# Performance work log

Hardware: AMD Instinct MI355X
Metric: run time of the kernel (lower is better)

## Reference

```python
import jax, jax.numpy as jnp
import numpy as np

N_NODES = 50000
N_EDGES = 800000
N_GRAPHS = 64
IN_CH = 128
HID = [64, 128]
MLP_CH = [128, 64, 64, 64, 1]


def _glorot(key, fan_in, fan_out):
    lim = jnp.sqrt(6.0 / (fan_in + fan_out))
    return jax.random.uniform(key, (fan_in, fan_out), jnp.float32, -lim, lim)


def setup_inputs() -> dict:
    key = jax.random.key(0)
    ks = jax.random.split(key, 16)
    x = jax.random.normal(ks[0], (N_NODES, IN_CH), jnp.float32)
    edge_index = jax.random.randint(ks[1], (2, N_EDGES), 0, N_NODES, jnp.int64)
    batch = jnp.sort(jax.random.randint(ks[2], (N_NODES,), 0, N_GRAPHS, jnp.int64))
    inp = {"x": x, "edge_index": edge_index, "batch": batch}
    # GCNConv weights (x @ W + b)
    inp["W1"] = _glorot(ks[3], IN_CH, HID[0]);  inp["b1"] = jnp.zeros((HID[0],), jnp.float32)
    inp["W2"] = _glorot(ks[4], HID[0], HID[1]); inp["b2"] = jnp.zeros((HID[1],), jnp.float32)
    # MLP weights
    for i in range(4):
        inp[f"M{i+1}"] = _glorot(ks[5 + i], MLP_CH[i], MLP_CH[i + 1])
        inp[f"c{i+1}"] = jnp.zeros((MLP_CH[i + 1],), jnp.float32)
    return inp


def _gcn_conv(x, src, dst, dinv, W, b):
    # x' = D^-1/2 (A + I) D^-1/2 (x W) + b, via gather-scale-scatter over edges
    h = x @ W                                   # [N, F]
    norm = dinv[src] * dinv[dst]                # [E+N]
    msg = h[src] * norm[:, None]                # gather + scale
    out = jax.ops.segment_sum(msg, dst, num_segments=x.shape[0])
    return out + b


def reference(x, edge_index, batch, W1, b1, W2, b2, M1, c1, M2, c2, M3, c3, M4, c4):
    N = x.shape[0]
    x = x.astype(jnp.float32)
    # add self loops (PyG GCNConv default)
    loops = jnp.arange(N, dtype=edge_index.dtype)
    src = jnp.concatenate([edge_index[0], loops])
    dst = jnp.concatenate([edge_index[1], loops])
    deg = jax.ops.segment_sum(jnp.ones_like(src, jnp.float32), dst, num_segments=N)
    dinv = jnp.where(deg > 0, jax.lax.rsqrt(jnp.maximum(deg, 1.0)), 0.0)

    h = jax.nn.relu(_gcn_conv(x, src, dst, dinv, W1, b1))
    h = jax.nn.relu(_gcn_conv(h, src, dst, dinv, W2, b2))

    # global mean pool per graph
    sums = jax.ops.segment_sum(h, batch, num_segments=N_GRAPHS)
    cnts = jax.ops.segment_sum(jnp.ones((N,), jnp.float32), batch, num_segments=N_GRAPHS)
    g = sums / jnp.maximum(cnts, 1.0)[:, None]   # [G, 128]

    # MLP (eval mode: dropout is identity)
    g = jax.nn.leaky_relu(g @ M1 + c1, negative_slope=0.2)
    g = jax.nn.leaky_relu(g @ M2 + c2, negative_slope=0.1)
    g = jax.nn.leaky_relu(g @ M3 + c3, negative_slope=0.1)
    g = jax.nn.relu(g @ M4 + c4)
    return g
```

## Files before the change

### kernel.cpp

```cpp
#include <hip/hip_runtime.h>
#include <hip/hip_fp16.h>

#define N_NODES 50000
#define N_EDGES 800000
#define N_GRAPHS 64

#define CAP 64
#define FILL_STRIPES 256

struct __align__(8)  h4v { __half2 a, b; };
struct __align__(16) h8v { __half2 a, b, c, d; };


__global__ void k_init(int* __restrict__ cnt, float* __restrict__ sums,
                       const float* __restrict__ W2, __half* __restrict__ w2h,
                       const int* __restrict__ batch, int* __restrict__ gend) {
    int i = blockIdx.x * 256 + threadIdx.x;
    if (i < N_NODES) {
        cnt[i] = 0;
        if (i == N_NODES - 1 || batch[i] != batch[i + 1]) gend[batch[i]] = i + 1;
    }
    if (i < N_GRAPHS * 128) sums[i] = 0.f;
    if (i < 64 * 128) w2h[i] = __float2half_rn(W2[i]);
}


__global__ void k_fill_direct(const int* __restrict__ src, const int* __restrict__ dst,
                              int* __restrict__ cnt, unsigned short* __restrict__ csr, int E) {
    const int range = blockIdx.x & 7;
    const int stripe = blockIdx.x >> 3;
    const int lo = range * (N_NODES / 8);
    const int hi = lo + (N_NODES / 8);
    for (int e = stripe * 256 + threadIdx.x; e < E; e += FILL_STRIPES * 256) {
        int d = dst[e];
        if (d >= lo && d < hi) {
            int slot = atomicAdd(&cnt[d], 1);
            if (slot < CAP) csr[(size_t)d * CAP + slot] = (unsigned short)src[e];
        }
    }
}


__global__ __launch_bounds__(256) void k_gemm1(const float* __restrict__ A,
                                               const float* __restrict__ W,
                                               const int* __restrict__ cnt,
                                               __half* __restrict__ Cout, int N) {
    const int FIN = 128;
    __shared__ __align__(16) float As[64 * (FIN + 2)];
    __shared__ __align__(16) float Wsm[FIN * 64];
    const int t = threadIdx.x;
    const int row0 = blockIdx.x * 64;

    const int NF4 = 64 * FIN / 4;
    for (int idx = t; idx < NF4; idx += 256) {
        int r = idx / (FIN / 4);
        int c4 = idx % (FIN / 4);
        float4 v = make_float4(0.f, 0.f, 0.f, 0.f);
        if (row0 + r < N) v = ((const float4*)(A + (size_t)(row0 + r) * FIN))[c4];
        float* p = &As[r * (FIN + 2) + c4 * 4];
        ((float2*)p)[0] = make_float2(v.x, v.y);
        ((float2*)p)[1] = make_float2(v.z, v.w);
    }
    for (int idx = t; idx < FIN * 16; idx += 256) {
        int r = idx / 16, c4 = idx % 16;
        *((float4*)&Wsm[r * 64 + c4 * 4]) = ((const float4*)(W + (size_t)r * 64))[c4];
    }
    __syncthreads();

    const int tc = (t & 15) * 4;
    const int tr = (t >> 4) * 4;
    float acc[4][4] = {};
#pragma unroll 4
    for (int k = 0; k < FIN; k += 2) {
        float2 a[4];
#pragma unroll
        for (int r = 0; r < 4; ++r)
            a[r] = *(const float2*)&As[(tr + r) * (FIN + 2) + k];
        float4 w0 = *(const float4*)&Wsm[k * 64 + tc];
        float4 w1 = *(const float4*)&Wsm[(k + 1) * 64 + tc];
#pragma unroll
        for (int r = 0; r < 4; ++r) {
            acc[r][0] = fmaf(a[r].x, w0.x, acc[r][0]);
            acc[r][1] = fmaf(a[r].x, w0.y, acc[r][1]);
            acc[r][2] = fmaf(a[r].x, w0.z, acc[r][2]);
            acc[r][3] = fmaf(a[r].x, w0.w, acc[r][3]);
            acc[r][0] = fmaf(a[r].y, w1.x, acc[r][0]);
            acc[r][1] = fmaf(a[r].y, w1.y, acc[r][1]);
            acc[r][2] = fmaf(a[r].y, w1.z, acc[r][2]);
            acc[r][3] = fmaf(a[r].y, w1.w, acc[r][3]);
        }
    }

#pragma unroll
    for (int r = 0; r < 4; ++r) {
        int row = row0 + tr + r;
        if (row < N) {
            float s = rsqrtf((float)(min(cnt[row], CAP) + 1));
            __half2* dsth = (__half2*)(Cout + (size_t)row * 64 + tc);
            dsth[0] = __floats2half2_rn(acc[r][0] * s, acc[r][1] * s);
            dsth[1] = __floats2half2_rn(acc[r][2] * s, acc[r][3] * s);
        }
    }
}


template <bool RELU>
__global__ void k_agg(const h8v* __restrict__ h, const int* __restrict__ cnt,
                      const unsigned short* __restrict__ csr,
                      const float* __restrict__ bias, h8v* __restrict__ out, int N) {
    int node = blockIdx.x * 32 + (threadIdx.x >> 3);
    int lane = threadIdx.x & 7;
    if (node >= N) return;
    int c = min(cnt[node], CAP);
    float di = rsqrtf((float)(c + 1));
    h8v sv = h[(size_t)node * 8 + lane];
    float2 p0 = __half22float2(sv.a), p1 = __half22float2(sv.b);
    float2 p2 = __half22float2(sv.c), p3 = __half22float2(sv.d);
    float f0 = p0.x, f1 = p0.y, f2 = p1.x, f3 = p1.y;
    float f4 = p2.x, f5 = p2.y, f6 = p3.x, f7 = p3.y;
    float g0 = 0, g1 = 0, g2 = 0, g3 = 0, g4 = 0, g5 = 0, g6 = 0, g7 = 0;
    const unsigned short* row = csr + (size_t)node * CAP;
    int j = 0;
    for (; j + 4 <= c; j += 4) {
        ushort4 s4 = *(const ushort4*)(row + j);
        h8v v0 = h[(size_t)s4.x * 8 + lane];
        h8v v1 = h[(size_t)s4.y * 8 + lane];
        h8v v2 = h[(size_t)s4.z * 8 + lane];
        h8v v3 = h[(size_t)s4.w * 8 + lane];
        float2 a0 = __half22float2(v0.a), a1 = __half22float2(v0.b),
               a2 = __half22float2(v0.c), a3 = __half22float2(v0.d);
        float2 b0 = __half22float2(v1.a), b1 = __half22float2(v1.b),
               b2 = __half22float2(v1.c), b3 = __half22float2(v1.d);
        f0 += a0.x; f1 += a0.y; f2 += a1.x; f3 += a1.y;
        f4 += a2.x; f5 += a2.y; f6 += a3.x; f7 += a3.y;
        g0 += b0.x; g1 += b0.y; g2 += b1.x; g3 += b1.y;
        g4 += b2.x; g5 += b2.y; g6 += b3.x; g7 += b3.y;
        float2 c0 = __half22float2(v2.a), c1 = __half22float2(v2.b),
               c2 = __half22float2(v2.c), c3 = __half22float2(v2.d);
        float2 d0 = __half22float2(v3.a), d1 = __half22float2(v3.b),
               d2 = __half22float2(v3.c), d3 = __half22float2(v3.d);
        f0 += c0.x; f1 += c0.y; f2 += c1.x; f3 += c1.y;
        f4 += c2.x; f5 += c2.y; f6 += c3.x; f7 += c3.y;
        g0 += d0.x; g1 += d0.y; g2 += d1.x; g3 += d1.y;
        g4 += d2.x; g5 += d2.y; g6 += d3.x; g7 += d3.y;
    }
    for (; j < c; ++j) {
        h8v v = h[(size_t)row[j] * 8 + lane];
        float2 a0 = __half22float2(v.a), a1 = __half22float2(v.b),
               a2 = __half22float2(v.c), a3 = __half22float2(v.d);
        f0 += a0.x; f1 += a0.y; f2 += a1.x; f3 += a1.y;
        f4 += a2.x; f5 += a2.y; f6 += a3.x; f7 += a3.y;
    }
    float s0 = f0 + g0, s1 = f1 + g1, s2 = f2 + g2, s3 = f3 + g3;
    float s4 = f4 + g4, s5 = f5 + g5, s6 = f6 + g6, s7 = f7 + g7;
    h8v o;
    if (RELU) {
        float4 bv0 = ((const float4*)bias)[lane * 2];
        float4 bv1 = ((const float4*)bias)[lane * 2 + 1];
        float r0 = fmaf(s0, di, bv0.x); r0 = r0 > 0.f ? r0 : 0.f;
        float r1 = fmaf(s1, di, bv0.y); r1 = r1 > 0.f ? r1 : 0.f;
        float r2 = fmaf(s2, di, bv0.z); r2 = r2 > 0.f ? r2 : 0.f;
        float r3 = fmaf(s3, di, bv0.w); r3 = r3 > 0.f ? r3 : 0.f;
        float r4 = fmaf(s4, di, bv1.x); r4 = r4 > 0.f ? r4 : 0.f;
        float r5 = fmaf(s5, di, bv1.y); r5 = r5 > 0.f ? r5 : 0.f;
        float r6 = fmaf(s6, di, bv1.z); r6 = r6 > 0.f ? r6 : 0.f;
        float r7 = fmaf(s7, di, bv1.w); r7 = r7 > 0.f ? r7 : 0.f;
        o.a = __floats2half2_rn(di * r0, di * r1);
        o.b = __floats2half2_rn(di * r2, di * r3);
        o.c = __floats2half2_rn(di * r4, di * r5);
        o.d = __floats2half2_rn(di * r6, di * r7);
    } else {
        o.a = __floats2half2_rn(s0 * di, s1 * di);
        o.b = __floats2half2_rn(s2 * di, s3 * di);
        o.c = __floats2half2_rn(s4 * di, s5 * di);
        o.d = __floats2half2_rn(s6 * di, s7 * di);
    }
    out[(size_t)node * 8 + lane] = o;
}


__global__ __launch_bounds__(256) void k_gemm_pool128(
    const __half2* __restrict__ A2,
    const __half2* __restrict__ w2h,
    const float* __restrict__ bias,
    const int* __restrict__ batch,
    float* __restrict__ sums, int N) {
    __shared__ __align__(16) float As[64 * 66];
    __shared__ __align__(16) __half2 Wh[64 * 64];
    __shared__ float red[8][132];
    __shared__ int batchLDS[64];
    const int t = threadIdx.x;
    const int row0 = blockIdx.x * 64;

    for (int idx = t; idx < 4096; idx += 256) Wh[idx] = w2h[idx];
    if (t < 64) batchLDS[t] = batch[min(row0 + t, N - 1)];
    for (int idx = t; idx < 64 * 32; idx += 256) {
        int r = idx >> 5, c2 = idx & 31;
        float2 v = make_float2(0.f, 0.f);
        if (row0 + r < N) v = __half22float2(A2[(size_t)(row0 + r) * 32 + c2]);
        *(float2*)&As[r * 66 + c2 * 2] = v;
    }
    __syncthreads();

    const int tc = (t & 31) * 4;
    const int tr = (t >> 5) * 8;
    float acc[8][4] = {};
#pragma unroll 4
    for (int k = 0; k < 64; k += 2) {
        float2 a[8];
#pragma unroll
        for (int r = 0; r < 8; ++r)
            a[r] = *(const float2*)&As[(tr + r) * 66 + k];
        h4v wv0 = *(const h4v*)&Wh[k * 64 + (tc >> 1)];
        h4v wv1 = *(const h4v*)&Wh[(k + 1) * 64 + (tc >> 1)];
        float2 w00 = __half22float2(wv0.a), w01 = __half22float2(wv0.b);
        float2 w10 = __half22float2(wv1.a), w11 = __half22float2(wv1.b);
#pragma unroll
        for (int r = 0; r < 8; ++r) {
            acc[r][0] = fmaf(a[r].x, w00.x, acc[r][0]);
            acc[r][1] = fmaf(a[r].x, w00.y, acc[r][1]);
            acc[r][2] = fmaf(a[r].x, w01.x, acc[r][2]);
            acc[r][3] = fmaf(a[r].x, w01.y, acc[r][3]);
            acc[r][0] = fmaf(a[r].y, w10.x, acc[r][0]);
            acc[r][1] = fmaf(a[r].y, w10.y, acc[r][1]);
            acc[r][2] = fmaf(a[r].y, w11.x, acc[r][2]);
            acc[r][3] = fmaf(a[r].y, w11.y, acc[r][3]);
        }
    }

    float4 bv = *(const float4*)&bias[tc];
    float v[8][4];
#pragma unroll
    for (int r = 0; r < 8; ++r) {
        bool valid = (row0 + tr + r) < N;
        v[r][0] = valid ? fmaxf(acc[r][0] + bv.x, 0.f) : 0.f;
        v[r][1] = valid ? fmaxf(acc[r][1] + bv.y, 0.f) : 0.f;
        v[r][2] = valid ? fmaxf(acc[r][2] + bv.z, 0.f) : 0.f;
        v[r][3] = valid ? fmaxf(acc[r][3] + bv.w, 0.f) : 0.f;
    }

    const int g0 = batchLDS[0], g1 = batchLDS[63];
    const int rg = t >> 5;
    for (int g = g0; g <= g1; ++g) {
        float p0 = 0.f, p1 = 0.f, p2 = 0.f, p3 = 0.f;
#pragma unroll
        for (int r = 0; r < 8; ++r) {
            if (batchLDS[tr + r] == g) { p0 += v[r][0]; p1 += v[r][1]; p2 += v[r][2]; p3 += v[r][3]; }
        }
        red[rg][tc + 0] = p0; red[rg][tc + 1] = p1;
        red[rg][tc + 2] = p2; red[rg][tc + 3] = p3;
        __syncthreads();
        for (int off = 4; off > 0; off >>= 1) {
            if (rg < off) {
#pragma unroll
                for (int c = 0; c < 4; ++c) red[rg][tc + c] += red[rg + off][tc + c];
            }
            __syncthreads();
        }
        if (rg == 0) {
#pragma unroll
            for (int c = 0; c < 4; ++c)
                atomicAdd(&sums[g * 128 + tc + c], red[0][tc + c]);
        }
        __syncthreads();
    }
}


__global__ void k_mlp(const float* __restrict__ sums, const int* __restrict__ gend,
                      const float* __restrict__ M1, const float* __restrict__ c1,
                      const float* __restrict__ M2, const float* __restrict__ c2,
                      const float* __restrict__ M3, const float* __restrict__ c3,
                      const float* __restrict__ M4, const float* __restrict__ c4,
                      float* __restrict__ out) {
    __shared__ float g[128], t1[64], t2[64], t3[64];
    __shared__ float cntb;
    int b = blockIdx.x;
    int t = threadIdx.x;
    if (t == 0) {
        int lb = (b > 0) ? gend[b - 1] : 0;
        cntb = fmaxf((float)(gend[b] - lb), 1.0f);
    }
    __syncthreads();
    if (t < 128) g[t] = sums[b * 128 + t] / cntb;
    __syncthreads();
    if (t < 64) {
        float acc = c1[t];
        for (int k = 0; k < 128; ++k) acc = fmaf(g[k], M1[k * 64 + t], acc);
        t1[t] = acc >= 0.f ? acc : 0.2f * acc;
    }
    __syncthreads();
    if (t < 64) {
        float acc = c2[t];
        for (int k = 0; k < 64; ++k) acc = fmaf(t1[k], M2[k * 64 + t], acc);
        t2[t] = acc >= 0.f ? acc : 0.1f * acc;
    }
    __syncthreads();
    if (t < 64) {
        float acc = c3[t];
        for (int k = 0; k < 64; ++k) acc = fmaf(t2[k], M3[k * 64 + t], acc);
        t3[t] = acc >= 0.f ? acc : 0.1f * acc;
    }
    __syncthreads();
    if (t == 0) {
        float acc = c4[0];
        for (int k = 0; k < 64; ++k) acc = fmaf(t3[k], M4[k], acc);
        out[b] = fmaxf(acc, 0.f);
    }
}


extern "C" void kernel_launch(void* const* d_in, const int* in_sizes, int n_in,
                              void* d_out, int out_size, void* d_ws, size_t ws_size,
                              hipStream_t stream) {
    const float* x   = (const float*)d_in[0];
    const int*   ei  = (const int*)d_in[1];
    const int*   bat = (const int*)d_in[2];
    const float* W1  = (const float*)d_in[3];
    const float* b1  = (const float*)d_in[4];
    const float* W2  = (const float*)d_in[5];
    const float* b2  = (const float*)d_in[6];
    const float* M1  = (const float*)d_in[7];
    const float* c1  = (const float*)d_in[8];
    const float* M2  = (const float*)d_in[9];
    const float* c2  = (const float*)d_in[10];
    const float* M3  = (const float*)d_in[11];
    const float* c3  = (const float*)d_in[12];
    const float* M4  = (const float*)d_in[13];
    const float* c4  = (const float*)d_in[14];
    float* out = (float*)d_out;

    const int* src = ei;
    const int* dst = ei + N_EDGES;

    float* bufA    = (float*)d_ws;
    float* bufB    = bufA + (size_t)N_NODES * 64;
    float* sums    = bufB + (size_t)N_NODES * 64;
    int*   cnt     = (int*)(sums + N_GRAPHS * 128);
    unsigned short* csr = (unsigned short*)(cnt + N_NODES);
    __half* w2h    = (__half*)(csr + (size_t)N_NODES * CAP);
    int*   gend    = (int*)(w2h + 64 * 128);

    k_init<<<(N_NODES + 255) / 256, 256, 0, stream>>>(cnt, sums, W2, w2h, bat, gend);
    k_fill_direct<<<8 * FILL_STRIPES, 256, 0, stream>>>(src, dst, cnt, csr, N_EDGES);

    const int NBLK = (N_NODES + 63) / 64;
    const int ABLK = (N_NODES + 31) / 32;

    k_gemm1<<<NBLK, 256, 0, stream>>>(x, W1, cnt, (__half*)bufA, N_NODES);
    k_agg<true><<<ABLK, 256, 0, stream>>>(
        (const h8v*)bufA, cnt, csr, b1, (h8v*)bufB, N_NODES);

    k_agg<false><<<ABLK, 256, 0, stream>>>(
        (const h8v*)bufB, cnt, csr, nullptr, (h8v*)bufA, N_NODES);
    k_gemm_pool128<<<NBLK, 256, 0, stream>>>(
        (const __half2*)bufA, (const __half2*)w2h, b2, bat, sums, N_NODES);

    k_mlp<<<N_GRAPHS, 128, 0, stream>>>(sums, gend,
                                        M1, c1, M2, c2, M3, c3, M4, c4, out);
}
```

Before: 216.2 us.

## Fuse init with CSR fill and pooling with MLP via cooperative grid sync

Merges the init kernel and the edge-fill kernel into one cooperative kernel that separates the two phases with a grid-wide sync. It also merges the GEMM-plus-pool kernel with the MLP head, so the first 64 blocks run the MLP after a grid sync. This removes two kernel launches and their inter-kernel gaps. In exchange it adds grid-barrier overhead and depends on every block being co-resident, which the launch-bounds occupancy hints are meant to guarantee; if that fails, the cooperative launch fails.

```diff
diff --git a/kernel.cpp b/kernel.cpp
--- a/kernel.cpp
+++ b/kernel.cpp
@@ -1,37 +1,41 @@
 #include <hip/hip_runtime.h>
 #include <hip/hip_fp16.h>
+#include <hip/hip_cooperative_groups.h>
+
+namespace cg = cooperative_groups;
 
 #define N_NODES 50000
 #define N_EDGES 800000
 #define N_GRAPHS 64
 
 #define CAP 64
-#define FILL_STRIPES 256
+#define BUILD_BLOCKS 2048
 
 struct __align__(8)  h4v { __half2 a, b; };
 struct __align__(16) h8v { __half2 a, b, c, d; };
 
 
-__global__ void k_init(int* __restrict__ cnt, float* __restrict__ sums,
-                       const float* __restrict__ W2, __half* __restrict__ w2h,
-                       const int* __restrict__ batch, int* __restrict__ gend) {
-    int i = blockIdx.x * 256 + threadIdx.x;
-    if (i < N_NODES) {
-        cnt[i] = 0;
-        if (i == N_NODES - 1 || batch[i] != batch[i + 1]) gend[batch[i]] = i + 1;
-    }
-    if (i < N_GRAPHS * 128) sums[i] = 0.f;
-    if (i < 64 * 128) w2h[i] = __float2half_rn(W2[i]);
-}
-
-
-__global__ void k_fill_direct(const int* __restrict__ src, const int* __restrict__ dst,
-                              int* __restrict__ cnt, unsigned short* __restrict__ csr, int E) {
+__global__ __launch_bounds__(256, 8) void k_build(
+    const int* __restrict__ src, const int* __restrict__ dst,
+    int* __restrict__ cnt, float* __restrict__ sums,
+    const float* __restrict__ W2, __half* __restrict__ w2h,
+    const int* __restrict__ batch, int* __restrict__ gend,
+    unsigned short* __restrict__ csr) {
+    const int tid = blockIdx.x * 256 + threadIdx.x;
+    if (tid < N_NODES) {
+        cnt[tid] = 0;
+        if (tid == N_NODES - 1 || batch[tid] != batch[tid + 1]) gend[batch[tid]] = tid + 1;
+    }
+    if (tid < N_GRAPHS * 128) sums[tid] = 0.f;
+    if (tid < 64 * 128) w2h[tid] = __float2half_rn(W2[tid]);
+
+    cg::this_grid().sync();
+
     const int range = blockIdx.x & 7;
     const int stripe = blockIdx.x >> 3;
     const int lo = range * (N_NODES / 8);
     const int hi = lo + (N_NODES / 8);
-    for (int e = stripe * 256 + threadIdx.x; e < E; e += FILL_STRIPES * 256) {
+    for (int e = stripe * 256 + threadIdx.x; e < N_EDGES; e += (BUILD_BLOCKS / 8) * 256) {
         int d = dst[e];
         if (d >= lo && d < hi) {
             int slot = atomicAdd(&cnt[d], 1);
@@ -179,16 +183,24 @@
 }
 
 
-__global__ __launch_bounds__(256) void k_gemm_pool128(
+__global__ __launch_bounds__(256, 4) void k_poolmlp(
     const __half2* __restrict__ A2,
     const __half2* __restrict__ w2h,
     const float* __restrict__ bias,
     const int* __restrict__ batch,
-    float* __restrict__ sums, int N) {
+    float* __restrict__ sums, int N,
+    const int* __restrict__ gend,
+    const float* __restrict__ M1, const float* __restrict__ c1,
+    const float* __restrict__ M2, const float* __restrict__ c2,
+    const float* __restrict__ M3, const float* __restrict__ c3,
+    const float* __restrict__ M4, const float* __restrict__ c4,
+    float* __restrict__ out) {
     __shared__ __align__(16) float As[64 * 66];
     __shared__ __align__(16) __half2 Wh[64 * 64];
     __shared__ float red[8][132];
     __shared__ int batchLDS[64];
+    __shared__ float gv[128], t1[64], t2[64], t3[64];
+    __shared__ float cntb;
     const int t = threadIdx.x;
     const int row0 = blockIdx.x * 64;
 
@@ -204,108 +216,103 @@
 
     const int tc = (t & 31) * 4;
     const int tr = (t >> 5) * 8;
-    float acc[8][4] = {};
+    {
+        float acc[8][4] = {};
 #pragma unroll 4
-    for (int k = 0; k < 64; k += 2) {
-        float2 a[8];
-#pragma unroll
-        for (int r = 0; r < 8; ++r)
-            a[r] = *(const float2*)&As[(tr + r) * 66 + k];
-        h4v wv0 = *(const h4v*)&Wh[k * 64 + (tc >> 1)];
-        h4v wv1 = *(const h4v*)&Wh[(k + 1) * 64 + (tc >> 1)];
-        float2 w00 = __half22float2(wv0.a), w01 = __half22float2(wv0.b);
-        float2 w10 = __half22float2(wv1.a), w11 = __half22float2(wv1.b);
+        for (int k = 0; k < 64; k += 2) {
+            float2 a[8];
+#pragma unroll
+            for (int r = 0; r < 8; ++r)
+                a[r] = *(const float2*)&As[(tr + r) * 66 + k];
+            h4v wv0 = *(const h4v*)&Wh[k * 64 + (tc >> 1)];
+            h4v wv1 = *(const h4v*)&Wh[(k + 1) * 64 + (tc >> 1)];
+            float2 w00 = __half22float2(wv0.a), w01 = __half22float2(wv0.b);
+            float2 w10 = __half22float2(wv1.a), w11 = __half22float2(wv1.b);
+#pragma unroll
+            for (int r = 0; r < 8; ++r) {
+                acc[r][0] = fmaf(a[r].x, w00.x, acc[r][0]);
+                acc[r][1] = fmaf(a[r].x, w00.y, acc[r][1]);
+                acc[r][2] = fmaf(a[r].x, w01.x, acc[r][2]);
+                acc[r][3] = fmaf(a[r].x, w01.y, acc[r][3]);
+                acc[r][0] = fmaf(a[r].y, w10.x, acc[r][0]);
+                acc[r][1] = fmaf(a[r].y, w10.y, acc[r][1]);
+                acc[r][2] = fmaf(a[r].y, w11.x, acc[r][2]);
+                acc[r][3] = fmaf(a[r].y, w11.y, acc[r][3]);
+            }
+        }
+
+        float4 bv = *(const float4*)&bias[tc];
+        float v[8][4];
 #pragma unroll
         for (int r = 0; r < 8; ++r) {
-            acc[r][0] = fmaf(a[r].x, w00.x, acc[r][0]);
-            acc[r][1] = fmaf(a[r].x, w00.y, acc[r][1]);
-            acc[r][2] = fmaf(a[r].x, w01.x, acc[r][2]);
-            acc[r][3] = fmaf(a[r].x, w01.y, acc[r][3]);
-            acc[r][0] = fmaf(a[r].y, w10.x, acc[r][0]);
-            acc[r][1] = fmaf(a[r].y, w10.y, acc[r][1]);
-            acc[r][2] = fmaf(a[r].y, w11.x, acc[r][2]);
-            acc[r][3] = fmaf(a[r].y, w11.y, acc[r][3]);
-        }
-    }
-
-    float4 bv = *(const float4*)&bias[tc];
-    float v[8][4];
-#pragma unroll
-    for (int r = 0; r < 8; ++r) {
-        bool valid = (row0 + tr + r) < N;
-        v[r][0] = valid ? fmaxf(acc[r][0] + bv.x, 0.f) : 0.f;
-        v[r][1] = valid ? fmaxf(acc[r][1] + bv.y, 0.f) : 0.f;
-        v[r][2] = valid ? fmaxf(acc[r][2] + bv.z, 0.f) : 0.f;
-        v[r][3] = valid ? fmaxf(acc[r][3] + bv.w, 0.f) : 0.f;
-    }
-
-    const int g0 = batchLDS[0], g1 = batchLDS[63];
-    const int rg = t >> 5;
-    for (int g = g0; g <= g1; ++g) {
-        float p0 = 0.f, p1 = 0.f, p2 = 0.f, p3 = 0.f;
-#pragma unroll
-        for (int r = 0; r < 8; ++r) {
-            if (batchLDS[tr + r] == g) { p0 += v[r][0]; p1 += v[r][1]; p2 += v[r][2]; p3 += v[r][3]; }
-        }
-        red[rg][tc + 0] = p0; red[rg][tc + 1] = p1;
-        red[rg][tc + 2] = p2; red[rg][tc + 3] = p3;
-        __syncthreads();
-        for (int off = 4; off > 0; off >>= 1) {
-            if (rg < off) {
-#pragma unroll
-                for (int c = 0; c < 4; ++c) red[rg][tc + c] += red[rg + off][tc + c];
+            bool valid = (row0 + tr + r) < N;
+            v[r][0] = valid ? fmaxf(acc[r][0] + bv.x, 0.f) : 0.f;
+            v[r][1] = valid ? fmaxf(acc[r][1] + bv.y, 0.f) : 0.f;
+            v[r][2] = valid ? fmaxf(acc[r][2] + bv.z, 0.f) : 0.f;
+            v[r][3] = valid ? fmaxf(acc[r][3] + bv.w, 0.f) : 0.f;
+        }
+
+        const int g0 = batchLDS[0], g1 = batchLDS[63];
+        const int rg = t >> 5;
+        for (int g = g0; g <= g1; ++g) {
+            float p0 = 0.f, p1 = 0.f, p2 = 0.f, p3 = 0.f;
+#pragma unroll
+            for (int r = 0; r < 8; ++r) {
+                if (batchLDS[tr + r] == g) { p0 += v[r][0]; p1 += v[r][1]; p2 += v[r][2]; p3 += v[r][3]; }
+            }
+            red[rg][tc + 0] = p0; red[rg][tc + 1] = p1;
+            red[rg][tc + 2] = p2; red[rg][tc + 3] = p3;
+            __syncthreads();
+            for (int off = 4; off > 0; off >>= 1) {
+                if (rg < off) {
+#pragma unroll
+                    for (int c = 0; c < 4; ++c) red[rg][tc + c] += red[rg + off][tc + c];
+                }
+                __syncthreads();
+            }
+            if (rg == 0) {
+#pragma unroll
+                for (int c = 0; c < 4; ++c)
+                    atomicAdd(&sums[g * 128 + tc + c], red[0][tc + c]);
             }
             __syncthreads();
         }
-        if (rg == 0) {
-#pragma unroll
-            for (int c = 0; c < 4; ++c)
-                atomicAdd(&sums[g * 128 + tc + c], red[0][tc + c]);
-        }
-        __syncthreads();
-    }
-}
-
-
-__global__ void k_mlp(const float* __restrict__ sums, const int* __restrict__ gend,
-                      const float* __restrict__ M1, const float* __restrict__ c1,
-                      const float* __restrict__ M2, const float* __restrict__ c2,
-                      const float* __restrict__ M3, const float* __restrict__ c3,
-                      const float* __restrict__ M4, const float* __restrict__ c4,
-                      float* __restrict__ out) {
-    __shared__ float g[128], t1[64], t2[64], t3[64];
-    __shared__ float cntb;
-    int b = blockIdx.x;
-    int t = threadIdx.x;
-    if (t == 0) {
-        int lb = (b > 0) ? gend[b - 1] : 0;
-        cntb = fmaxf((float)(gend[b] - lb), 1.0f);
-    }
-    __syncthreads();
-    if (t < 128) g[t] = sums[b * 128 + t] / cntb;
-    __syncthreads();
-    if (t < 64) {
-        float acc = c1[t];
-        for (int k = 0; k < 128; ++k) acc = fmaf(g[k], M1[k * 64 + t], acc);
-        t1[t] = acc >= 0.f ? acc : 0.2f * acc;
-    }
-    __syncthreads();
-    if (t < 64) {
-        float acc = c2[t];
-        for (int k = 0; k < 64; ++k) acc = fmaf(t1[k], M2[k * 64 + t], acc);
-        t2[t] = acc >= 0.f ? acc : 0.1f * acc;
-    }
-    __syncthreads();
-    if (t < 64) {
-        float acc = c3[t];
-        for (int k = 0; k < 64; ++k) acc = fmaf(t2[k], M3[k * 64 + t], acc);
-        t3[t] = acc >= 0.f ? acc : 0.1f * acc;
-    }
-    __syncthreads();
-    if (t == 0) {
-        float acc = c4[0];
-        for (int k = 0; k < 64; ++k) acc = fmaf(t3[k], M4[k], acc);
-        out[b] = fmaxf(acc, 0.f);
+    }
+
+    cg::this_grid().sync();
+
+    if (blockIdx.x < N_GRAPHS) {
+        int b = blockIdx.x;
+        if (t == 0) {
+            int lb = (b > 0) ? gend[b - 1] : 0;
+            cntb = fmaxf((float)(gend[b] - lb), 1.0f);
+        }
+        __syncthreads();
+        if (t < 128) gv[t] = sums[b * 128 + t] / cntb;
+        __syncthreads();
+        if (t < 64) {
+            float acc = c1[t];
+            for (int k = 0; k < 128; ++k) acc = fmaf(gv[k], M1[k * 64 + t], acc);
+            t1[t] = acc >= 0.f ? acc : 0.2f * acc;
+        }
+        __syncthreads();
+        if (t < 64) {
+            float acc = c2[t];
+            for (int k = 0; k < 64; ++k) acc = fmaf(t1[k], M2[k * 64 + t], acc);
+            t2[t] = acc >= 0.f ? acc : 0.1f * acc;
+        }
+        __syncthreads();
+        if (t < 64) {
+            float acc = c3[t];
+            for (int k = 0; k < 64; ++k) acc = fmaf(t2[k], M3[k * 64 + t], acc);
+            t3[t] = acc >= 0.f ? acc : 0.1f * acc;
+        }
+        __syncthreads();
+        if (t == 0) {
+            float acc = c4[0];
+            for (int k = 0; k < 64; ++k) acc = fmaf(t3[k], M4[k], acc);
+            out[b] = fmaxf(acc, 0.f);
+        }
     }
 }
 
@@ -341,8 +348,12 @@
     __half* w2h    = (__half*)(csr + (size_t)N_NODES * CAP);
     int*   gend    = (int*)(w2h + 64 * 128);
 
-    k_init<<<(N_NODES + 255) / 256, 256, 0, stream>>>(cnt, sums, W2, w2h, bat, gend);
-    k_fill_direct<<<8 * FILL_STRIPES, 256, 0, stream>>>(src, dst, cnt, csr, N_EDGES);
+    {
+        void* args[] = {(void*)&src, (void*)&dst, (void*)&cnt, (void*)&sums,
+                        (void*)&W2, (void*)&w2h, (void*)&bat, (void*)&gend, (void*)&csr};
+        hipLaunchCooperativeKernel((const void*)k_build, dim3(BUILD_BLOCKS), dim3(256),
+                                   args, 0, stream);
+    }
 
     const int NBLK = (N_NODES + 63) / 64;
     const int ABLK = (N_NODES + 31) / 32;
@@ -353,9 +364,15 @@
 
     k_agg<false><<<ABLK, 256, 0, stream>>>(
         (const h8v*)bufB, cnt, csr, nullptr, (h8v*)bufA, N_NODES);
-    k_gemm_pool128<<<NBLK, 256, 0, stream>>>(
-        (const __half2*)bufA, (const __half2*)w2h, b2, bat, sums, N_NODES);
-
-    k_mlp<<<N_GRAPHS, 128, 0, stream>>>(sums, gend,
-                                        M1, c1, M2, c2, M3, c3, M4, c4, out);
-}
+    {
+        const __half2* A2 = (const __half2*)bufA;
+        const __half2* w2h2 = (const __half2*)w2h;
+        int N = N_NODES;
+        void* args[] = {(void*)&A2, (void*)&w2h2, (void*)&b2, (void*)&bat,
+                        (void*)&sums, (void*)&N, (void*)&gend,
+                        (void*)&M1, (void*)&c1, (void*)&M2, (void*)&c2,
+                        (void*)&M3, (void*)&c3, (void*)&M4, (void*)&c4, (void*)&out};
+        hipLaunchCooperativeKernel((const void*)k_poolmlp, dim3(NBLK), dim3(256),
+                                   args, 0, stream);
+    }
+}
```

Result: slower. 389.6 us (+80.2%).

## Fuse MLP head into pooling GEMM kernel using last-block ticket counter

Applied to the files above, without the earlier changes.

Removes the separate k_mlp launch. Each block of the pooling GEMM kernel takes a ticket from a global atomic counter. The last 64 blocks to finish spin-wait until every block has contributed, then each runs the MLP for one graph. This saves one kernel launch and its gap, at the cost of spin-waiting blocks and an extra counter reset in k_init.

```diff
diff --git a/kernel.cpp b/kernel.cpp
--- a/kernel.cpp
+++ b/kernel.cpp
@@ -7,6 +7,7 @@
 
 #define CAP 64
 #define FILL_STRIPES 256
+#define NBLK 782
 
 struct __align__(8)  h4v { __half2 a, b; };
 struct __align__(16) h8v { __half2 a, b, c, d; };
@@ -14,8 +15,10 @@
 
 __global__ void k_init(int* __restrict__ cnt, float* __restrict__ sums,
                        const float* __restrict__ W2, __half* __restrict__ w2h,
-                       const int* __restrict__ batch, int* __restrict__ gend) {
+                       const int* __restrict__ batch, int* __restrict__ gend,
+                       int* __restrict__ done) {
     int i = blockIdx.x * 256 + threadIdx.x;
+    if (i == 0) *done = 0;
     if (i < N_NODES) {
         cnt[i] = 0;
         if (i == N_NODES - 1 || batch[i] != batch[i + 1]) gend[batch[i]] = i + 1;
@@ -184,11 +187,18 @@
     const __half2* __restrict__ w2h,
     const float* __restrict__ bias,
     const int* __restrict__ batch,
-    float* __restrict__ sums, int N) {
+    float* __restrict__ sums, int N,
+    int* __restrict__ done, const int* __restrict__ gend,
+    const float* __restrict__ M1, const float* __restrict__ c1,
+    const float* __restrict__ M2, const float* __restrict__ c2,
+    const float* __restrict__ M3, const float* __restrict__ c3,
+    const float* __restrict__ M4, const float* __restrict__ c4,
+    float* __restrict__ out) {
     __shared__ __align__(16) float As[64 * 66];
     __shared__ __align__(16) __half2 Wh[64 * 64];
     __shared__ float red[8][132];
     __shared__ int batchLDS[64];
+    __shared__ int ticket;
     const int t = threadIdx.x;
     const int row0 = blockIdx.x * 64;
 
@@ -204,89 +214,98 @@
 
     const int tc = (t & 31) * 4;
     const int tr = (t >> 5) * 8;
-    float acc[8][4] = {};
+    {
+        float acc[8][4] = {};
 #pragma unroll 4
-    for (int k = 0; k < 64; k += 2) {
-        float2 a[8];
-#pragma unroll
-        for (int r = 0; r < 8; ++r)
-            a[r] = *(const float2*)&As[(tr + r) * 66 + k];
-        h4v wv0 = *(const h4v*)&Wh[k * 64 + (tc >> 1)];
-        h4v wv1 = *(const h4v*)&Wh[(k + 1) * 64 + (tc >> 1)];
-        float2 w00 = __half22float2(wv0.a), w01 = __half22float2(wv0.b);
-        float2 w10 = __half22float2(wv1.a), w11 = __half22float2(wv1.b);
+        for (int k = 0; k < 64; k += 2) {
+            float2 a[8];
+#pragma unroll
+            for (int r = 0; r < 8; ++r)
+                a[r] = *(const float2*)&As[(tr + r) * 66 + k];
+            h4v wv0 = *(const h4v*)&Wh[k * 64 + (tc >> 1)];
+            h4v wv1 = *(const h4v*)&Wh[(k + 1) * 64 + (tc >> 1)];
+            float2 w00 = __half22float2(wv0.a), w01 = __half22float2(wv0.b);
+            float2 w10 = __half22float2(wv1.a), w11 = __half22float2(wv1.b);
+#pragma unroll
+            for (int r = 0; r < 8; ++r) {
+                acc[r][0] = fmaf(a[r].x, w00.x, acc[r][0]);
+                acc[r][1] = fmaf(a[r].x, w00.y, acc[r][1]);
+                acc[r][2] = fmaf(a[r].x, w01.x, acc[r][2]);
+                acc[r][3] = fmaf(a[r].x, w01.y, acc[r][3]);
+                acc[r][0] = fmaf(a[r].y, w10.x, acc[r][0]);
+                acc[r][1] = fmaf(a[r].y, w10.y, acc[r][1]);
+                acc[r][2] = fmaf(a[r].y, w11.x, acc[r][2]);
+                acc[r][3] = fmaf(a[r].y, w11.y, acc[r][3]);
+            }
+        }
+
+        float4 bv = *(const float4*)&bias[tc];
+        float v[8][4];
 #pragma unroll
         for (int r = 0; r < 8; ++r) {
-            acc[r][0] = fmaf(a[r].x, w00.x, acc[r][0]);
-            acc[r][1] = fmaf(a[r].x, w00.y, acc[r][1]);
-            acc[r][2] = fmaf(a[r].x, w01.x, acc[r][2]);
-            acc[r][3] = fmaf(a[r].x, w01.y, acc[r][3]);
-            acc[r][0] = fmaf(a[r].y, w10.x, acc[r][0]);
-            acc[r][1] = fmaf(a[r].y, w10.y, acc[r][1]);
-            acc[r][2] = fmaf(a[r].y, w11.x, acc[r][2]);
-            acc[r][3] = fmaf(a[r].y, w11.y, acc[r][3]);
-        }
-    }
-
-    float4 bv = *(const float4*)&bias[tc];
-    float v[8][4];
-#pragma unroll
-    for (int r = 0; r < 8; ++r) {
-        bool valid = (row0 + tr + r) < N;
-        v[r][0] = valid ? fmaxf(acc[r][0] + bv.x, 0.f) : 0.f;
-        v[r][1] = valid ? fmaxf(acc[r][1] + bv.y, 0.f) : 0.f;
-        v[r][2] = valid ? fmaxf(acc[r][2] + bv.z, 0.f) : 0.f;
-        v[r][3] = valid ? fmaxf(acc[r][3] + bv.w, 0.f) : 0.f;
-    }
-
-    const int g0 = batchLDS[0], g1 = batchLDS[63];
-    const int rg = t >> 5;
-    for (int g = g0; g <= g1; ++g) {
-        float p0 = 0.f, p1 = 0.f, p2 = 0.f, p3 = 0.f;
-#pragma unroll
-        for (int r = 0; r < 8; ++r) {
-            if (batchLDS[tr + r] == g) { p0 += v[r][0]; p1 += v[r][1]; p2 += v[r][2]; p3 += v[r][3]; }
-        }
-        red[rg][tc + 0] = p0; red[rg][tc + 1] = p1;
-        red[rg][tc + 2] = p2; red[rg][tc + 3] = p3;
-        __syncthreads();
-        for (int off = 4; off > 0; off >>= 1) {
-            if (rg < off) {
-#pragma unroll
-                for (int c = 0; c < 4; ++c) red[rg][tc + c] += red[rg + off][tc + c];
+            bool valid = (row0 + tr + r) < N;
+            v[r][0] = valid ? fmaxf(acc[r][0] + bv.x, 0.f) : 0.f;
+            v[r][1] = valid ? fmaxf(acc[r][1] + bv.y, 0.f) : 0.f;
+            v[r][2] = valid ? fmaxf(acc[r][2] + bv.z, 0.f) : 0.f;
+            v[r][3] = valid ? fmaxf(acc[r][3] + bv.w, 0.f) : 0.f;
+        }
+
+        const int g0 = batchLDS[0], g1 = batchLDS[63];
+        const int rg = t >> 5;
+        for (int g = g0; g <= g1; ++g) {
+            float p0 = 0.f, p1 = 0.f, p2 = 0.f, p3 = 0.f;
+#pragma unroll
+            for (int r = 0; r < 8; ++r) {
+                if (batchLDS[tr + r] == g) { p0 += v[r][0]; p1 += v[r][1]; p2 += v[r][2]; p3 += v[r][3]; }
+            }
+            red[rg][tc + 0] = p0; red[rg][tc + 1] = p1;
+            red[rg][tc + 2] = p2; red[rg][tc + 3] = p3;
+            __syncthreads();
+            for (int off = 4; off > 0; off >>= 1) {
+                if (rg < off) {
+#pragma unroll
+                    for (int c = 0; c < 4; ++c) red[rg][tc + c] += red[rg + off][tc + c];
+                }
+                __syncthreads();
+            }
+            if (rg == 0) {
+#pragma unroll
+                for (int c = 0; c < 4; ++c)
+                    atomicAdd(&sums[g * 128 + tc + c], red[0][tc + c]);
             }
             __syncthreads();
         }
-        if (rg == 0) {
-#pragma unroll
-            for (int c = 0; c < 4; ++c)
-                atomicAdd(&sums[g * 128 + tc + c], red[0][tc + c]);
-        }
-        __syncthreads();
-    }
-}
-
-
-__global__ void k_mlp(const float* __restrict__ sums, const int* __restrict__ gend,
-                      const float* __restrict__ M1, const float* __restrict__ c1,
-                      const float* __restrict__ M2, const float* __restrict__ c2,
-                      const float* __restrict__ M3, const float* __restrict__ c3,
-                      const float* __restrict__ M4, const float* __restrict__ c4,
-                      float* __restrict__ out) {
-    __shared__ float g[128], t1[64], t2[64], t3[64];
-    __shared__ float cntb;
-    int b = blockIdx.x;
-    int t = threadIdx.x;
+    }
+
+    __threadfence();
+    __syncthreads();
+    if (t == 0) ticket = atomicAdd(done, 1);
+    __syncthreads();
+    const int tk = ticket;
+    if (tk < NBLK - N_GRAPHS) return;
+    const int b = tk - (NBLK - N_GRAPHS);
+
+    if (t == 0) {
+        while (atomicAdd(done, 0) < NBLK) __builtin_amdgcn_s_sleep(8);
+    }
+    __syncthreads();
+    __threadfence();
+
+    float* gv = As;
+    float* t1 = As + 128;
+    float* t2 = As + 192;
+    float* t3 = As + 256;
+    float* cntb = As + 320;
     if (t == 0) {
         int lb = (b > 0) ? gend[b - 1] : 0;
-        cntb = fmaxf((float)(gend[b] - lb), 1.0f);
-    }
-    __syncthreads();
-    if (t < 128) g[t] = sums[b * 128 + t] / cntb;
+        cntb[0] = fmaxf((float)(gend[b] - lb), 1.0f);
+    }
+    __syncthreads();
+    if (t < 128) gv[t] = atomicAdd(&sums[b * 128 + t], 0.f) / cntb[0];
     __syncthreads();
     if (t < 64) {
         float acc = c1[t];
-        for (int k = 0; k < 128; ++k) acc = fmaf(g[k], M1[k * 64 + t], acc);
+        for (int k = 0; k < 128; ++k) acc = fmaf(gv[k], M1[k * 64 + t], acc);
         t1[t] = acc >= 0.f ? acc : 0.2f * acc;
     }
     __syncthreads();
@@ -340,11 +359,11 @@
     unsigned short* csr = (unsigned short*)(cnt + N_NODES);
     __half* w2h    = (__half*)(csr + (size_t)N_NODES * CAP);
     int*   gend    = (int*)(w2h + 64 * 128);
-
-    k_init<<<(N_NODES + 255) / 256, 256, 0, stream>>>(cnt, sums, W2, w2h, bat, gend);
+    int*   done    = gend + 64;
+
+    k_init<<<(N_NODES + 255) / 256, 256, 0, stream>>>(cnt, sums, W2, w2h, bat, gend, done);
     k_fill_direct<<<8 * FILL_STRIPES, 256, 0, stream>>>(src, dst, cnt, csr, N_EDGES);
 
-    const int NBLK = (N_NODES + 63) / 64;
     const int ABLK = (N_NODES + 31) / 32;
 
     k_gemm1<<<NBLK, 256, 0, stream>>>(x, W1, cnt, (__half*)bufA, N_NODES);
@@ -354,8 +373,6 @@
     k_agg<false><<<ABLK, 256, 0, stream>>>(
         (const h8v*)bufB, cnt, csr, nullptr, (h8v*)bufA, N_NODES);
     k_gemm_pool128<<<NBLK, 256, 0, stream>>>(
-        (const __half2*)bufA, (const __half2*)w2h, b2, bat, sums, N_NODES);
-
-    k_mlp<<<N_GRAPHS, 128, 0, stream>>>(sums, gend,
-                                        M1, c1, M2, c2, M3, c3, M4, c4, out);
-}
+        (const __half2*)bufA, (const __half2*)w2h, b2, bat, sums, N_NODES,
+        done, gend, M1, c1, M2, c2, M3, c3, M4, c4, out);
+}
```

Result: slower. 263.9 us (+22.1%).
